# Performance work log

Hardware: AMD Instinct MI355X
Metric: run time of the kernel (lower is better)

## Reference

```python
import jax, jax.numpy as jnp
import numpy as np

N_NODES = 100000
N_EDGES = 600000
N_FEAT = 128
DIM = 128
N_LAYERS = 4
N_GRAPHS = 1000
BN_EPS = 1e-4


def setup_inputs() -> dict:
    key = jax.random.key(0)
    ks = jax.random.split(key, 12)
    s = 0.05
    x = jax.random.normal(ks[0], (N_NODES, N_FEAT), dtype=jnp.float32)
    edge_index = jax.random.randint(ks[1], (2, N_EDGES), 0, N_NODES, dtype=jnp.int64)
    batch = jnp.sort(jax.random.randint(ks[2], (N_NODES,), 0, N_GRAPHS, dtype=jnp.int64))
    pre_w = jax.random.normal(ks[3], (N_FEAT, DIM), dtype=jnp.float32) * s
    pre_b = jnp.zeros((DIM,), dtype=jnp.float32)
    # GIN MLP weights (first layer input is DIM since pre projects to DIM)
    conv_w1 = jax.random.normal(ks[4], (N_LAYERS, DIM, DIM), dtype=jnp.float32) * s
    conv_w2 = jax.random.normal(ks[5], (N_LAYERS, DIM, DIM), dtype=jnp.float32) * s
    bn_g = jnp.ones((N_LAYERS, DIM), dtype=jnp.float32)
    bn_b = jnp.zeros((N_LAYERS, DIM), dtype=jnp.float32)
    ed = DIM * N_LAYERS  # embedding_dim = 512
    ff_w1 = jax.random.normal(ks[6], (ed, ed), dtype=jnp.float32) * s
    ff_w2 = jax.random.normal(ks[7], (ed, ed), dtype=jnp.float32) * s
    ff_w3 = jax.random.normal(ks[8], (ed, ed), dtype=jnp.float32) * s
    ff_sc = jax.random.normal(ks[9], (ed, ed), dtype=jnp.float32) * s
    return dict(x=x, edge_index=edge_index, batch=batch, pre_w=pre_w, pre_b=pre_b,
                conv_w1=conv_w1, conv_w2=conv_w2, bn_g=bn_g, bn_b=bn_b,
                ff_w1=ff_w1, ff_w2=ff_w2, ff_w3=ff_w3, ff_sc=ff_sc)


def reference(x, edge_index, batch, pre_w, pre_b, conv_w1, conv_w2, bn_g, bn_b,
              ff_w1, ff_w2, ff_w3, ff_sc):
    lrelu = jax.nn.leaky_relu  # negative_slope=0.01 matches torch default
    n = x.shape[0]
    src, dst = edge_index[0], edge_index[1]

    h = x @ pre_w + pre_b  # [N, DIM]
    xs = []
    for i in range(conv_w1.shape[0]):
        # GINConv (eps=0): nn(x + sum_{j->i} x_j); gather at src, scatter-add at dst
        agg = jax.ops.segment_sum(h[src], dst, num_segments=n)
        h2 = h + agg
        h2 = lrelu(h2 @ conv_w1[i]) @ conv_w2[i]
        # BatchNorm1d (training mode, biased variance, eps=1e-4)
        mean = jnp.mean(h2, axis=0)
        var = jnp.var(h2, axis=0)
        h = (h2 - mean) * jax.lax.rsqrt(var + BN_EPS) * bn_g[i] + bn_b[i]
        xs.append(h)

    # global_add_pool per layer, then concat -> [G, DIM*L]
    pooled = [jax.ops.segment_sum(hl, batch, num_segments=N_GRAPHS) for hl in xs]
    y = jnp.concatenate(pooled, axis=1)

    z = lrelu(lrelu(lrelu(y @ ff_w1) @ ff_w2) @ ff_w3) + y @ ff_sc
    return z
```

## Files before the change

### kernel.cpp

```cpp
#include <hip/hip_runtime.h>
#include <hip/hip_bf16.h>

typedef __hip_bfloat16 bf16;
typedef unsigned int u32;
typedef __attribute__((ext_vector_type(8))) short short8v;
typedef __attribute__((ext_vector_type(4))) float f32x4;

__device__ __forceinline__ float lrelu_f(float v) { return v > 0.f ? v : 0.01f * v; }
__device__ __forceinline__ float bf_lo(u32 u) { return __uint_as_float(u << 16); }
__device__ __forceinline__ float bf_hi(u32 u) { return __uint_as_float(u & 0xffff0000u); }
__device__ __forceinline__ unsigned short bbits(float v) {
    union { bf16 b; unsigned short s; } u; u.b = __float2bfloat16(v); return u.s;
}
__device__ __forceinline__ u32 pack2(float a, float b) {
    return (u32)bbits(a) | ((u32)bbits(b) << 16);
}
__device__ __forceinline__ float ld_ext(const void* p, size_t idx, int f32f) {
    return f32f ? ((const float*)p)[idx] : __bfloat162float(((const bf16*)p)[idx]);
}

__global__ void probe_k(const int* __restrict__ ei, const int* __restrict__ batch,
                        const u32* __restrict__ bng, int nedges, int nnodes,
                        int* __restrict__ flags, float* __restrict__ scaleA,
                        float* __restrict__ shiftA)
{
    __shared__ int nz[2];
    if (threadIdx.x < 2) nz[threadIdx.x] = 0;
    __syncthreads();
    int t = threadIdx.x;
    if (ei[(nedges + 2 * t) | 1] != 0) atomicAdd(&nz[0], 1);
    if (batch[((nnodes >> 1) + 2 * t) | 1] != 0) atomicAdd(&nz[1], 1);
    if (t < 128) { scaleA[t] = 1.f; shiftA[t] = 0.f; }
    __syncthreads();
    if (t == 0) {
        flags[0] = (nz[0] == 0) ? 1 : 0;
        flags[1] = (nz[1] == 0) ? 1 : 0;
        flags[2] = (bng[0] == 0x3F800000u) ? 1 : 0;
    }
}

__global__ __launch_bounds__(256)
void hist_k(const int* __restrict__ ei, int* __restrict__ deg, int nedges,
            const int* __restrict__ flags)
{
    int e = blockIdx.x * 256 + threadIdx.x;
    if (e >= nedges) return;
    int f = flags[0];
    int dst = f ? ei[(nedges + e) << 1] : ei[nedges + e];
    atomicAdd(&deg[dst], 1);
}

__global__ __launch_bounds__(256)
void scan1_k(const int* __restrict__ deg, int* __restrict__ bsum, int n)
{
    __shared__ int l[256];
    int t = threadIdx.x, i = blockIdx.x * 256 + t;
    l[t] = (i < n) ? deg[i] : 0;
    __syncthreads();
    for (int off = 128; off > 0; off >>= 1) {
        if (t < off) l[t] += l[t + off];
        __syncthreads();
    }
    if (t == 0) bsum[blockIdx.x] = l[0];
}
__global__ __launch_bounds__(1024)
void scan2_k(int* __restrict__ bsum, int nb)
{
    __shared__ int l[1024];
    int t = threadIdx.x;
    int orig = (t < nb) ? bsum[t] : 0;
    l[t] = orig;
    __syncthreads();
    for (int off = 1; off < 1024; off <<= 1) {
        int v = (t >= off) ? l[t - off] : 0;
        __syncthreads();
        l[t] += v;
        __syncthreads();
    }
    if (t < nb) bsum[t] = l[t] - orig;
}
__global__ __launch_bounds__(256)
void scan3_k(const int* __restrict__ deg, const int* __restrict__ bsum,
             int* __restrict__ rowptr, int* __restrict__ cursor, int n)
{
    __shared__ int l[256];
    int t = threadIdx.x, i = blockIdx.x * 256 + t;
    int d = (i < n) ? deg[i] : 0;
    l[t] = d;
    __syncthreads();
    for (int off = 1; off < 256; off <<= 1) {
        int v = (t >= off) ? l[t - off] : 0;
        __syncthreads();
        l[t] += v;
        __syncthreads();
    }
    int excl = l[t] - d + bsum[blockIdx.x];
    if (i < n) {
        rowptr[i] = excl;
        cursor[i] = excl;
        if (i == n - 1) rowptr[n] = excl + d;
    }
}

__global__ __launch_bounds__(256)
void fill_k(const int* __restrict__ ei, int* __restrict__ cursor,
            int* __restrict__ srcs, int nedges, const int* __restrict__ flags)
{
    int e = blockIdx.x * 256 + threadIdx.x;
    if (e >= nedges) return;
    int f = flags[0];
    int src = ei[e << f];
    int dst = f ? ei[(nedges + e) << 1] : ei[nedges + e];
    int pos = atomicAdd(&cursor[dst], 1);
    srcs[pos] = src;
}

__global__ __launch_bounds__(256)
void wprep_k(const void* __restrict__ W, bf16* __restrict__ Wf,
             int K, int N, int L, int wstride, const int* __restrict__ flags)
{
    int e = blockIdx.x * 256 + threadIdx.x;
    int PL = K * N;
    if (e >= L * PL) return;
    int l = e / PL, r = e % PL;
    int KS = K >> 5;
    int j = r & 7, lane = (r >> 3) & 63;
    int rem = r >> 9;
    int ks = rem % KS, nt = rem / KS;
    int k = ks * 32 + ((lane >> 4) << 3) + j;
    int n = nt * 16 + (lane & 15);
    Wf[e] = __float2bfloat16(ld_ext(W, (size_t)(l * K + k) * wstride + n, flags[2]));
}

template<int SRC, int MODE, int OBF>
__global__ __launch_bounds__(256)
void mgemm_k(const void* __restrict__ A, const bf16* __restrict__ Wf,
             const void* __restrict__ bias, void* __restrict__ out,
             int nrows, int K, int astride, int ostride, const int* __restrict__ flags)
{
    const int KS = K >> 5;
    const int t = threadIdx.x, w = t >> 6, lane = t & 63;
    const int quad = lane >> 4, lr = lane & 15;
    const int rbase = blockIdx.x * 64 + w * 16;
    const int arow = min(rbase + lr, nrows - 1);
    const int ntg0 = blockIdx.y * 8;
    const int f32f = flags[2];

    f32x4 acc[8];
    #pragma unroll
    for (int i = 0; i < 8; ++i) acc[i] = (f32x4){0.f, 0.f, 0.f, 0.f};

    for (int ks = 0; ks < KS; ++ks) {
        const int kof = ks * 32 + quad * 8;
        short8v a;
        if (SRC == 0 || f32f) {
            const float* Af = (const float*)A + (size_t)arow * astride + kof;
            float4 p0 = *(const float4*)Af;
            float4 p1 = *(const float4*)(Af + 4);
            a[0] = (short)bbits(p0.x); a[1] = (short)bbits(p0.y);
            a[2] = (short)bbits(p0.z); a[3] = (short)bbits(p0.w);
            a[4] = (short)bbits(p1.x); a[5] = (short)bbits(p1.y);
            a[6] = (short)bbits(p1.z); a[7] = (short)bbits(p1.w);
        } else {
            a = *(const short8v*)((const short*)A + (size_t)arow * astride + kof);
        }
        #pragma unroll
        for (int nt = 0; nt < 8; ++nt) {
            const short8v b = *(const short8v*)&Wf[(((size_t)(ntg0 + nt) * KS + ks) * 64 + lane) * 8];
            acc[nt] = __builtin_amdgcn_mfma_f32_16x16x32_bf16(a, b, acc[nt], 0, 0, 0);
        }
    }

    #pragma unroll
    for (int nt = 0; nt < 8; ++nt) {
        const int col = (ntg0 + nt) * 16 + lr;
        float bv = 0.f;
        if (MODE == 0 && bias != nullptr) bv = ld_ext(bias, col, f32f);
        #pragma unroll
        for (int r = 0; r < 4; ++r) {
            int orow = rbase + quad * 4 + r;
            if (orow < nrows) {
                float v = acc[nt][r] + bv;
                if (MODE == 1) v = lrelu_f(v);
                if (OBF) ((bf16*)out)[(size_t)orow * ostride + col] = __float2bfloat16(v);
                else     ((float*)out)[(size_t)orow * ostride + col] = v;
            }
        }
    }
}

__global__ __launch_bounds__(256)
void conv_k(const u32* __restrict__ aggb, const bf16* __restrict__ Wf1,
            const bf16* __restrict__ Wf2, u32* __restrict__ h2,
            float* __restrict__ psum, float* __restrict__ psq, int nrows)
{
    __shared__ bf16 tls[4][16][136];
    __shared__ float lsum[128], lsq[128];
    const int t = threadIdx.x, w = t >> 6, lane = t & 63;
    const int quad = lane >> 4, lr = lane & 15;
    const int rbase = blockIdx.x * 64 + w * 16;
    const int arow = min(rbase + lr, nrows - 1);
    if (t < 128) { lsum[t] = 0.f; lsq[t] = 0.f; }

    f32x4 acc[8];
    #pragma unroll
    for (int i = 0; i < 8; ++i) acc[i] = (f32x4){0.f, 0.f, 0.f, 0.f};
    #pragma unroll
    for (int ks = 0; ks < 4; ++ks) {
        short8v a = *(const short8v*)&aggb[(size_t)arow * 64 + ks * 16 + quad * 4];
        #pragma unroll
        for (int nt = 0; nt < 8; ++nt) {
            const short8v b = *(const short8v*)&Wf1[((nt * 4 + ks) * 64 + lane) * 8];
            acc[nt] = __builtin_amdgcn_mfma_f32_16x16x32_bf16(a, b, acc[nt], 0, 0, 0);
        }
    }
    #pragma unroll
    for (int nt = 0; nt < 8; ++nt)
        #pragma unroll
        for (int r = 0; r < 4; ++r)
            tls[w][quad * 4 + r][nt * 16 + lr] = __float2bfloat16(lrelu_f(acc[nt][r]));
    __syncthreads();

    f32x4 acc2[8];
    #pragma unroll
    for (int i = 0; i < 8; ++i) acc2[i] = (f32x4){0.f, 0.f, 0.f, 0.f};
    #pragma unroll
    for (int ks = 0; ks < 4; ++ks) {
        short8v a = *(const short8v*)&tls[w][lr][ks * 32 + quad * 8];
        #pragma unroll
        for (int nt = 0; nt < 8; ++nt) {
            const short8v b = *(const short8v*)&Wf2[((nt * 4 + ks) * 64 + lane) * 8];
            acc2[nt] = __builtin_amdgcn_mfma_f32_16x16x32_bf16(a, b, acc2[nt], 0, 0, 0);
        }
    }
    #pragma unroll
    for (int nt = 0; nt < 8; ++nt) {
        float s = 0.f, q = 0.f;
        #pragma unroll
        for (int r = 0; r < 4; ++r) {
            int orow = rbase + quad * 4 + r;
            if (orow < nrows) {
                float v = acc2[nt][r];
                s += v; q += v * v;
                ((bf16*)h2)[(size_t)orow * 128 + nt * 16 + lr] = __float2bfloat16(v);
            }
        }
        atomicAdd(&lsum[nt * 16 + lr], s);
        atomicAdd(&lsq[nt * 16 + lr], q);
    }
    __syncthreads();
    if (t < 128) {
        psum[(size_t)blockIdx.x * 128 + t] = lsum[t];
        psq[(size_t)blockIdx.x * 128 + t] = lsq[t];
    }
}

__global__ __launch_bounds__(256)
void reduce_bn_k(const float* __restrict__ psum, const float* __restrict__ psq,
                 const void* __restrict__ g, const void* __restrict__ b,
                 float* __restrict__ scale, float* __restrict__ shift,
                 float inv_n, int layer, int nblk, const int* __restrict__ flags)
{
    __shared__ float ls[256], lq[256];
    int c = blockIdx.x, t = threadIdx.x;
    float s = 0.f, q = 0.f;
    for (int i = t; i < nblk; i += 256) {
        s += psum[(size_t)i * 128 + c];
        q += psq[(size_t)i * 128 + c];
    }
    ls[t] = s; lq[t] = q;
    __syncthreads();
    for (int off = 128; off > 0; off >>= 1) {
        if (t < off) { ls[t] += ls[t + off]; lq[t] += lq[t + off]; }
        __syncthreads();
    }
    if (t == 0) {
        int f32f = flags[2];
        size_t off = (size_t)layer * 128 + c;
        float mean = ls[0] * inv_n;
        float var = lq[0] * inv_n - mean * mean;
        float sc = ld_ext(g, off, f32f) * rsqrtf(fmaxf(var, 0.f) + 1e-4f);
        scale[c] = sc;
        shift[c] = ld_ext(b, off, f32f) - mean * sc;
    }
}

__global__ __launch_bounds__(256)
void aggregate_k(const int* __restrict__ rowptr, const int* __restrict__ srcs,
                 const u32* __restrict__ h2, u32* __restrict__ aggb,
                 const float* __restrict__ scale, const float* __restrict__ shift, int nnodes)
{
    int node = blockIdx.x * 4 + (threadIdx.x >> 6);
    if (node >= nnodes) return;
    int lane = threadIdx.x & 63;
    u32 u = h2[(size_t)node * 64 + lane];
    float ax = bf_lo(u), ay = bf_hi(u);
    int lo = rowptr[node], hi = rowptr[node + 1];
    int e = lo;
    for (; e + 4 <= hi; e += 4) {
        int s0 = srcs[e], s1 = srcs[e + 1], s2 = srcs[e + 2], s3 = srcs[e + 3];
        u32 v0 = h2[(size_t)s0 * 64 + lane];
        u32 v1 = h2[(size_t)s1 * 64 + lane];
        u32 v2 = h2[(size_t)s2 * 64 + lane];
        u32 v3 = h2[(size_t)s3 * 64 + lane];
        ax += bf_lo(v0) + bf_lo(v1) + bf_lo(v2) + bf_lo(v3);
        ay += bf_hi(v0) + bf_hi(v1) + bf_hi(v2) + bf_hi(v3);
    }
    for (; e < hi; ++e) {
        u32 v = h2[(size_t)srcs[e] * 64 + lane];
        ax += bf_lo(v);
        ay += bf_hi(v);
    }
    float cnt = (float)(hi - lo + 1);
    int c = lane * 2;
    float r0 = fmaf(ax, scale[c], shift[c] * cnt);
    float r1 = fmaf(ay, scale[c + 1], shift[c + 1] * cnt);
    aggb[(size_t)node * 64 + lane] = pack2(r0, r1);
}

__device__ __forceinline__ int lower_bound_b(const int* b, int n, int key, int fb)
{
    int lo = 0, hi = n;
    while (lo < hi) {
        int m = (lo + hi) >> 1;
        if (b[m << fb] < key) lo = m + 1; else hi = m;
    }
    return lo;
}

__global__ __launch_bounds__(64)
void pool_k(const u32* __restrict__ h2, const int* __restrict__ batch,
            float* __restrict__ y, int layer, int nnodes,
            const float* __restrict__ scale, const float* __restrict__ shift,
            const int* __restrict__ flags)
{
    int g = blockIdx.x, t = threadIdx.x;
    int fb = flags[1];
    int lo = lower_bound_b(batch, nnodes, g, fb);
    int hi = lower_bound_b(batch, nnodes, g + 1, fb);
    float s0 = 0.f, s1 = 0.f;
    int i = lo;
    for (; i + 4 <= hi; i += 4) {
        u32 u0 = h2[(size_t)i * 64 + t];
        u32 u1 = h2[(size_t)(i + 1) * 64 + t];
        u32 u2 = h2[(size_t)(i + 2) * 64 + t];
        u32 u3 = h2[(size_t)(i + 3) * 64 + t];
        s0 += bf_lo(u0) + bf_lo(u1) + bf_lo(u2) + bf_lo(u3);
        s1 += bf_hi(u0) + bf_hi(u1) + bf_hi(u2) + bf_hi(u3);
    }
    for (; i < hi; ++i) {
        u32 u = h2[(size_t)i * 64 + t];
        s0 += bf_lo(u);
        s1 += bf_hi(u);
    }
    float cnt = (float)(hi - lo);
    int c = t * 2;
    float* yp = &y[(size_t)g * 512 + layer * 128 + c];
    yp[0] = fmaf(s0, scale[c], shift[c] * cnt);
    yp[1] = fmaf(s1, scale[c + 1], shift[c + 1] * cnt);
}

__global__ __launch_bounds__(256)
void final_k(const float* __restrict__ a, const float* __restrict__ b,
             float* __restrict__ out, int n)
{
    int i = blockIdx.x * 256 + threadIdx.x;
    if (i < n) out[i] = a[i] + b[i];
}

extern "C" void kernel_launch(void* const* d_in, const int* in_sizes, int n_in,
                              void* d_out, int out_size, void* d_ws, size_t ws_size,
                              hipStream_t stream)
{
    const void* x       = d_in[0];
    const int*  ei      = (const int*)d_in[1];
    const int*  batch   = (const int*)d_in[2];
    const void* pre_w   = d_in[3];
    const void* pre_b   = d_in[4];
    const void* conv_w1 = d_in[5];
    const void* conv_w2 = d_in[6];
    const void* bn_g    = d_in[7];
    const void* bn_b    = d_in[8];
    const void* ff_w[4] = { d_in[9], d_in[10], d_in[11], d_in[12] };

    const int n_nodes  = in_sizes[2];
    const int n_edges  = in_sizes[1] / 2;
    const int n_graphs = out_size / 512;
    const size_t nf = (size_t)n_nodes * 128;
    const int nsb = (n_nodes + 255) / 256;
    const int nblk = (n_nodes + 63) / 64;

    float* ws      = (float*)d_ws;
    int*   flags   = (int*)ws;
    int*   bsum    = (int*)(ws + 16);
    float* scaleA  = ws + 1056;
    float* shiftA  = scaleA + 5 * 128;
    float* psum    = shiftA + 5 * 128;
    float* psq     = psum + (size_t)nblk * 128;
    float* y       = psq + (size_t)nblk * 128;
    float* tA      = y  + (size_t)n_graphs * 512;
    float* tB      = tA + (size_t)n_graphs * 512;
    u32*   bufA    = (u32*)(tB + (size_t)n_graphs * 512);
    u32*   bufB    = bufA + nf / 2;
    int*   deg     = (int*)(bufB + nf / 2);
    int*   rowptr  = deg + n_nodes;
    int*   srcs    = rowptr + n_nodes + 1;
    bf16*  Wfn     = (bf16*)(((uintptr_t)(srcs + n_edges) + 15) & ~(uintptr_t)15);
    bf16*  Wff     = Wfn + 9 * 16384;

    probe_k<<<1, 256, 0, stream>>>(ei, batch, (const u32*)bn_g, n_edges, n_nodes,
                                   flags, scaleA, shiftA);

    hipMemsetAsync(deg, 0, n_nodes * sizeof(int), stream);
    hist_k<<<(n_edges + 255) / 256, 256, 0, stream>>>(ei, deg, n_edges, flags);
    scan1_k<<<nsb, 256, 0, stream>>>(deg, bsum, n_nodes);
    scan2_k<<<1, 1024, 0, stream>>>(bsum, nsb);
    scan3_k<<<nsb, 256, 0, stream>>>(deg, bsum, rowptr, deg, n_nodes);
    fill_k<<<(n_edges + 255) / 256, 256, 0, stream>>>(ei, deg, srcs, n_edges, flags);

    wprep_k<<<64, 256, 0, stream>>>(pre_w, Wfn, 128, 128, 1, 128, flags);
    wprep_k<<<256, 256, 0, stream>>>(conv_w1, Wfn + 16384, 128, 128, 4, 128, flags);
    wprep_k<<<256, 256, 0, stream>>>(conv_w2, Wfn + 5 * 16384, 128, 128, 4, 128, flags);
    for (int m = 0; m < 4; ++m)
        wprep_k<<<1024, 256, 0, stream>>>(ff_w[m], Wff + (size_t)m * 262144, 512, 512, 1, 512, flags);

    const dim3 gn(nblk, 1);
    const dim3 gf((n_graphs + 63) / 64, 4);

    mgemm_k<1, 0, 1><<<gn, 256, 0, stream>>>(x, Wfn, pre_b, bufA, n_nodes, 128, 128, 128, flags);

    for (int l = 0; l < 4; ++l) {
        const u32* src = (l & 1) ? bufB : bufA;
        u32*       dst = (l & 1) ? bufA : bufB;
        aggregate_k<<<(n_nodes + 3) / 4, 256, 0, stream>>>(
            rowptr, srcs, src, dst, scaleA + l * 128, shiftA + l * 128, n_nodes);
        conv_k<<<gn, 256, 0, stream>>>(dst, Wfn + (1 + l) * 16384, Wfn + (5 + l) * 16384,
                                       dst , psum, psq, n_nodes);
        reduce_bn_k<<<128, 256, 0, stream>>>(psum, psq, bn_g, bn_b,
                                             scaleA + (l + 1) * 128, shiftA + (l + 1) * 128,
                                             1.f / (float)n_nodes, l, nblk, flags);
        pool_k<<<n_graphs, 64, 0, stream>>>(dst, batch, y, l, n_nodes,
                                            scaleA + (l + 1) * 128, shiftA + (l + 1) * 128, flags);
    }

    mgemm_k<0, 0, 0><<<gf, 256, 0, stream>>>(y,  Wff + 3ull * 262144, nullptr, tB, n_graphs, 512, 512, 512, flags);
    mgemm_k<0, 1, 0><<<gf, 256, 0, stream>>>(y,  Wff + 0ull * 262144, nullptr, tA, n_graphs, 512, 512, 512, flags);
    mgemm_k<0, 1, 0><<<gf, 256, 0, stream>>>(tA, Wff + 1ull * 262144, nullptr, y,  n_graphs, 512, 512, 512, flags);
    mgemm_k<0, 1, 0><<<gf, 256, 0, stream>>>(y,  Wff + 2ull * 262144, nullptr, tA, n_graphs, 512, 512, 512, flags);

    final_k<<<(n_graphs * 512 + 255) / 256, 256, 0, stream>>>(tA, tB, (float*)d_out, n_graphs * 512);
}
```

Measured before the change: 869.5 us.

## Merge weight-prep launches, double conv rows per warp, pack pool graphs per block

All seven weight-preparation launches become one kernel that dispatches on the flat element index. The fused conv kernel now handles 32 rows per warp (128 per block), so each loaded weight fragment feeds two MFMAs and half as many BN partial sums are written. pool_k packs four graphs per 256-thread block instead of one graph per 64-thread block. Together these cut launch overhead and repeated weight loads. In exchange, conv uses more registers and LDS per block, which may lower occupancy.

```diff
diff --git a/kernel.cpp b/kernel.cpp
--- a/kernel.cpp
+++ b/kernel.cpp
@@ -116,13 +116,23 @@
 }
 
 __global__ __launch_bounds__(256)
-void wprep_k(const void* __restrict__ W, bf16* __restrict__ Wf,
-             int K, int N, int L, int wstride, const int* __restrict__ flags)
+void wprep_all_k(const void* __restrict__ pre_w, const void* __restrict__ w1,
+                 const void* __restrict__ w2, const void* __restrict__ f0,
+                 const void* __restrict__ f1, const void* __restrict__ f2,
+                 const void* __restrict__ f3, bf16* __restrict__ Wf,
+                 const int* __restrict__ flags)
 {
     int e = blockIdx.x * 256 + threadIdx.x;
-    int PL = K * N;
-    if (e >= L * PL) return;
-    int l = e / PL, r = e % PL;
+    if (e >= 1196032) return;
+    const void* W; int K, wstride, l, r;
+    if (e < 16384)       { W = pre_w; K = 128; wstride = 128; l = 0; r = e; }
+    else if (e < 81920)  { int q = e - 16384; W = w1; K = 128; wstride = 128; l = q >> 14; r = q & 16383; }
+    else if (e < 147456) { int q = e - 81920; W = w2; K = 128; wstride = 128; l = q >> 14; r = q & 16383; }
+    else {
+        int q = e - 147456; int m = q >> 18; r = q & 262143;
+        W = (m == 0) ? f0 : (m == 1) ? f1 : (m == 2) ? f2 : f3;
+        K = 512; wstride = 512; l = 0;
+    }
     int KS = K >> 5;
     int j = r & 7, lane = (r >> 3) & 63;
     int rem = r >> 9;
@@ -189,65 +199,79 @@
     }
 }
 
-__global__ __launch_bounds__(256)
+__global__ __launch_bounds__(256, 4)
 void conv_k(const u32* __restrict__ aggb, const bf16* __restrict__ Wf1,
             const bf16* __restrict__ Wf2, u32* __restrict__ h2,
             float* __restrict__ psum, float* __restrict__ psq, int nrows)
 {
-    __shared__ bf16 tls[4][16][136];
+    __shared__ bf16 tls[4][32][136];
     __shared__ float lsum[128], lsq[128];
     const int t = threadIdx.x, w = t >> 6, lane = t & 63;
     const int quad = lane >> 4, lr = lane & 15;
-    const int rbase = blockIdx.x * 64 + w * 16;
-    const int arow = min(rbase + lr, nrows - 1);
+    const int rbase = blockIdx.x * 128 + w * 32;
+    const int arow0 = min(rbase + lr, nrows - 1);
+    const int arow1 = min(rbase + 16 + lr, nrows - 1);
     if (t < 128) { lsum[t] = 0.f; lsq[t] = 0.f; }
 
-    f32x4 acc[8];
-    #pragma unroll
-    for (int i = 0; i < 8; ++i) acc[i] = (f32x4){0.f, 0.f, 0.f, 0.f};
+    f32x4 acc[2][8];
+    #pragma unroll
+    for (int h = 0; h < 2; ++h)
+        #pragma unroll
+        for (int i = 0; i < 8; ++i) acc[h][i] = (f32x4){0.f, 0.f, 0.f, 0.f};
+
     #pragma unroll
     for (int ks = 0; ks < 4; ++ks) {
-        short8v a = *(const short8v*)&aggb[(size_t)arow * 64 + ks * 16 + quad * 4];
+        short8v a0 = *(const short8v*)&aggb[(size_t)arow0 * 64 + ks * 16 + quad * 4];
+        short8v a1 = *(const short8v*)&aggb[(size_t)arow1 * 64 + ks * 16 + quad * 4];
         #pragma unroll
         for (int nt = 0; nt < 8; ++nt) {
             const short8v b = *(const short8v*)&Wf1[((nt * 4 + ks) * 64 + lane) * 8];
-            acc[nt] = __builtin_amdgcn_mfma_f32_16x16x32_bf16(a, b, acc[nt], 0, 0, 0);
-        }
-    }
-    #pragma unroll
-    for (int nt = 0; nt < 8; ++nt)
-        #pragma unroll
-        for (int r = 0; r < 4; ++r)
-            tls[w][quad * 4 + r][nt * 16 + lr] = __float2bfloat16(lrelu_f(acc[nt][r]));
-    __syncthreads();
-
-    f32x4 acc2[8];
-    #pragma unroll
-    for (int i = 0; i < 8; ++i) acc2[i] = (f32x4){0.f, 0.f, 0.f, 0.f};
+            acc[0][nt] = __builtin_amdgcn_mfma_f32_16x16x32_bf16(a0, b, acc[0][nt], 0, 0, 0);
+            acc[1][nt] = __builtin_amdgcn_mfma_f32_16x16x32_bf16(a1, b, acc[1][nt], 0, 0, 0);
+        }
+    }
+    #pragma unroll
+    for (int h = 0; h < 2; ++h)
+        #pragma unroll
+        for (int nt = 0; nt < 8; ++nt)
+            #pragma unroll
+            for (int r = 0; r < 4; ++r)
+                tls[w][h * 16 + quad * 4 + r][nt * 16 + lr] = __float2bfloat16(lrelu_f(acc[h][nt][r]));
+    __syncthreads();
+
+    f32x4 acc2[2][8];
+    #pragma unroll
+    for (int h = 0; h < 2; ++h)
+        #pragma unroll
+        for (int i = 0; i < 8; ++i) acc2[h][i] = (f32x4){0.f, 0.f, 0.f, 0.f};
     #pragma unroll
     for (int ks = 0; ks < 4; ++ks) {
-        short8v a = *(const short8v*)&tls[w][lr][ks * 32 + quad * 8];
+        short8v a0 = *(const short8v*)&tls[w][lr][ks * 32 + quad * 8];
+        short8v a1 = *(const short8v*)&tls[w][16 + lr][ks * 32 + quad * 8];
         #pragma unroll
         for (int nt = 0; nt < 8; ++nt) {
             const short8v b = *(const short8v*)&Wf2[((nt * 4 + ks) * 64 + lane) * 8];
-            acc2[nt] = __builtin_amdgcn_mfma_f32_16x16x32_bf16(a, b, acc2[nt], 0, 0, 0);
-        }
-    }
-    #pragma unroll
-    for (int nt = 0; nt < 8; ++nt) {
-        float s = 0.f, q = 0.f;
-        #pragma unroll
-        for (int r = 0; r < 4; ++r) {
-            int orow = rbase + quad * 4 + r;
-            if (orow < nrows) {
-                float v = acc2[nt][r];
-                s += v; q += v * v;
-                ((bf16*)h2)[(size_t)orow * 128 + nt * 16 + lr] = __float2bfloat16(v);
+            acc2[0][nt] = __builtin_amdgcn_mfma_f32_16x16x32_bf16(a0, b, acc2[0][nt], 0, 0, 0);
+            acc2[1][nt] = __builtin_amdgcn_mfma_f32_16x16x32_bf16(a1, b, acc2[1][nt], 0, 0, 0);
+        }
+    }
+    #pragma unroll
+    for (int h = 0; h < 2; ++h)
+        #pragma unroll
+        for (int nt = 0; nt < 8; ++nt) {
+            float s = 0.f, q = 0.f;
+            #pragma unroll
+            for (int r = 0; r < 4; ++r) {
+                int orow = rbase + h * 16 + quad * 4 + r;
+                if (orow < nrows) {
+                    float v = acc2[h][nt][r];
+                    s += v; q += v * v;
+                    ((bf16*)h2)[(size_t)orow * 128 + nt * 16 + lr] = __float2bfloat16(v);
+                }
             }
-        }
-        atomicAdd(&lsum[nt * 16 + lr], s);
-        atomicAdd(&lsq[nt * 16 + lr], q);
-    }
+            atomicAdd(&lsum[nt * 16 + lr], s);
+            atomicAdd(&lsq[nt * 16 + lr], q);
+        }
     __syncthreads();
     if (t < 128) {
         psum[(size_t)blockIdx.x * 128 + t] = lsum[t];
@@ -328,13 +352,15 @@
     return lo;
 }
 
-__global__ __launch_bounds__(64)
+__global__ __launch_bounds__(256)
 void pool_k(const u32* __restrict__ h2, const int* __restrict__ batch,
-            float* __restrict__ y, int layer, int nnodes,
+            float* __restrict__ y, int layer, int nnodes, int ngraphs,
             const float* __restrict__ scale, const float* __restrict__ shift,
             const int* __restrict__ flags)
 {
-    int g = blockIdx.x, t = threadIdx.x;
+    int g = blockIdx.x * 4 + (threadIdx.x >> 6);
+    if (g >= ngraphs) return;
+    int t = threadIdx.x & 63;
     int fb = flags[1];
     int lo = lower_bound_b(batch, nnodes, g, fb);
     int hi = lower_bound_b(batch, nnodes, g + 1, fb);
@@ -381,14 +407,13 @@
     const void* conv_w2 = d_in[6];
     const void* bn_g    = d_in[7];
     const void* bn_b    = d_in[8];
-    const void* ff_w[4] = { d_in[9], d_in[10], d_in[11], d_in[12] };
 
     const int n_nodes  = in_sizes[2];
     const int n_edges  = in_sizes[1] / 2;
     const int n_graphs = out_size / 512;
     const size_t nf = (size_t)n_nodes * 128;
     const int nsb = (n_nodes + 255) / 256;
-    const int nblk = (n_nodes + 63) / 64;
+    const int nblk = (n_nodes + 127) / 128;
 
     float* ws      = (float*)d_ws;
     int*   flags   = (int*)ws;
@@ -418,29 +443,28 @@
     scan3_k<<<nsb, 256, 0, stream>>>(deg, bsum, rowptr, deg, n_nodes);
     fill_k<<<(n_edges + 255) / 256, 256, 0, stream>>>(ei, deg, srcs, n_edges, flags);
 
-    wprep_k<<<64, 256, 0, stream>>>(pre_w, Wfn, 128, 128, 1, 128, flags);
-    wprep_k<<<256, 256, 0, stream>>>(conv_w1, Wfn + 16384, 128, 128, 4, 128, flags);
-    wprep_k<<<256, 256, 0, stream>>>(conv_w2, Wfn + 5 * 16384, 128, 128, 4, 128, flags);
-    for (int m = 0; m < 4; ++m)
-        wprep_k<<<1024, 256, 0, stream>>>(ff_w[m], Wff + (size_t)m * 262144, 512, 512, 1, 512, flags);
-
-    const dim3 gn(nblk, 1);
+    wprep_all_k<<<(1196032 + 255) / 256, 256, 0, stream>>>(
+        pre_w, conv_w1, conv_w2, d_in[9], d_in[10], d_in[11], d_in[12], Wfn, flags);
+
+    const dim3 gpre((n_nodes + 63) / 64, 1);
+    const dim3 gconv(nblk, 1);
     const dim3 gf((n_graphs + 63) / 64, 4);
 
-    mgemm_k<1, 0, 1><<<gn, 256, 0, stream>>>(x, Wfn, pre_b, bufA, n_nodes, 128, 128, 128, flags);
+    mgemm_k<1, 0, 1><<<gpre, 256, 0, stream>>>(x, Wfn, pre_b, bufA, n_nodes, 128, 128, 128, flags);
 
     for (int l = 0; l < 4; ++l) {
         const u32* src = (l & 1) ? bufB : bufA;
         u32*       dst = (l & 1) ? bufA : bufB;
         aggregate_k<<<(n_nodes + 3) / 4, 256, 0, stream>>>(
             rowptr, srcs, src, dst, scaleA + l * 128, shiftA + l * 128, n_nodes);
-        conv_k<<<gn, 256, 0, stream>>>(dst, Wfn + (1 + l) * 16384, Wfn + (5 + l) * 16384,
-                                       dst , psum, psq, n_nodes);
+        conv_k<<<gconv, 256, 0, stream>>>(dst, Wfn + (1 + l) * 16384, Wfn + (5 + l) * 16384,
+                                          dst , psum, psq, n_nodes);
         reduce_bn_k<<<128, 256, 0, stream>>>(psum, psq, bn_g, bn_b,
                                              scaleA + (l + 1) * 128, shiftA + (l + 1) * 128,
                                              1.f / (float)n_nodes, l, nblk, flags);
-        pool_k<<<n_graphs, 64, 0, stream>>>(dst, batch, y, l, n_nodes,
-                                            scaleA + (l + 1) * 128, shiftA + (l + 1) * 128, flags);
+        pool_k<<<(n_graphs + 3) / 4, 256, 0, stream>>>(
+            dst, batch, y, l, n_nodes, n_graphs,
+            scaleA + (l + 1) * 128, shiftA + (l + 1) * 128, flags);
     }
 
     mgemm_k<0, 0, 0><<<gf, 256, 0, stream>>>(y,  Wff + 3ull * 262144, nullptr, tB, n_graphs, 512, 512, 512, flags);
```

Measured after the change: 856.1 us. Within noise of the previous version (-1.5%).
